# Optimization experiments

Hardware: AMD Instinct MI355X
Metric: run time of the kernel (lower is better)

Reference implementation:

```python
import jax, jax.numpy as jnp
import numpy as np

N_HEAD = 16

def setup_inputs() -> dict:
    key = jax.random.key(0)
    ks = jax.random.split(key, 5)
    B, S, D = 4, 2048, 1024
    return {
        "string": jax.random.normal(ks[0], (B, S, D), dtype=jnp.float32),
        "string_len": jax.random.randint(ks[1], (B,), 1, S + 1),
        "Wqkv": jax.random.normal(ks[2], (D, 3 * D), dtype=jnp.float32) * 0.02,
        "bqkv": jnp.zeros((3 * D,), dtype=jnp.float32),
        "Wo": jax.random.normal(ks[3], (D, D), dtype=jnp.float32) * 0.02,
        "bo": jnp.zeros((D,), dtype=jnp.float32),
    }


def reference(string, string_len, Wqkv, bqkv, Wo, bo):
    B, S, D = string.shape
    H = N_HEAD
    hd = D // H
    x = string @ Wqkv + bqkv                      # [B,S,3D]
    q, k, v = jnp.split(x, 3, axis=-1)
    # split heads -> [B,H,S,hd]
    q = q.reshape(B, S, H, hd).transpose(0, 2, 1, 3)
    k = k.reshape(B, S, H, hd).transpose(0, 2, 1, 3)
    v = v.reshape(B, S, H, hd).transpose(0, 2, 1, 3)
    w = jnp.einsum('bhqd,bhkd->bhqk', q, k) / jnp.sqrt(jnp.float32(hd))
    causal = jnp.tril(jnp.ones((S, S), dtype=bool))  # [S,S]
    w = jnp.where(causal[None, None], w, jnp.float32(-1e9))
    w = jax.nn.softmax(w, axis=-1)
    a = jnp.einsum('bhqk,bhkd->bhqd', w, v)       # [B,H,S,hd]
    a = a.transpose(0, 2, 1, 3).reshape(B, S, D)  # merge heads
    a = a @ Wo + bo
    return a, string_len
```

## Files before the change

### kernel.cpp

```cpp
#include <hip/hip_runtime.h>
#include <stdint.h>

typedef __attribute__((ext_vector_type(8))) short bf16x8;
typedef __attribute__((ext_vector_type(4))) float f32x4;
typedef __attribute__((ext_vector_type(16))) float f32x16;
typedef __attribute__((ext_vector_type(4))) unsigned short u16x4;

static constexpr int Bn = 4, Sn = 2048, Dn = 1024, Hn = 16, HD = 64;
static constexpr int Mrows = Bn * Sn;
static constexpr int D3 = 3 * Dn;

__device__ __forceinline__ unsigned short f2bf(float f) {
  unsigned int u = __float_as_uint(f);
  u += 0x7FFF + ((u >> 16) & 1);
  return (unsigned short)(u >> 16);
}

__device__ __forceinline__ void gload16(const void* gptr, void* lptr) {
  __builtin_amdgcn_global_load_lds(
      (__attribute__((address_space(1))) void*)gptr,
      (__attribute__((address_space(3))) void*)lptr, 16, 0, 0);
}

__device__ __forceinline__ int swz8(int r) { return (r ^ (r >> 3)) & 7; }

__device__ __forceinline__ float vexp2(float x) {
#if __has_builtin(__builtin_amdgcn_exp2f)
  return __builtin_amdgcn_exp2f(x);
#else
  return exp2f(x);
#endif
}

__device__ __forceinline__ unsigned cvtpk(float lo, float hi) {
  unsigned r;
  asm("v_cvt_pk_bf16_f32 %0, %1, %2" : "=v"(r) : "v"(lo), "v"(hi));
  return r;
}

__device__ __forceinline__ float lanepull(float v, int srclane) {
  return __int_as_float(__builtin_amdgcn_ds_bpermute(srclane * 4, __float_as_int(v)));
}

__global__ void cvt_f32_bf16(const float* __restrict__ in,
                             unsigned short* __restrict__ out, int n) {
  int i = (blockIdx.x * blockDim.x + threadIdx.x) * 4;
  if (i < n) {
    const float4 v = *(const float4*)(in + i);
    u16x4 o;
    o.x = f2bf(v.x); o.y = f2bf(v.y); o.z = f2bf(v.z); o.w = f2bf(v.w);
    *(u16x4*)(out + i) = o;
  }
}

__global__ void transpose_cvt(const float* __restrict__ W,
                              unsigned short* __restrict__ Wt, int K, int N) {
  __shared__ float tile[32][33];
  const int n0 = blockIdx.x * 32, k0 = blockIdx.y * 32;
  const int tx = threadIdx.x, ty = threadIdx.y;
  #pragma unroll
  for (int j = 0; j < 4; j++)
    tile[ty + 8 * j][tx] = W[(size_t)(k0 + ty + 8 * j) * N + n0 + tx];
  __syncthreads();
  #pragma unroll
  for (int j = 0; j < 4; j++)
    Wt[(size_t)(n0 + ty + 8 * j) * K + k0 + tx] = f2bf(tile[tx][ty + 8 * j]);
}

template<bool BF16_OUT>
__global__ __launch_bounds__(512, 1)
void gemm_bt2(const unsigned short* __restrict__ A,
              const unsigned short* __restrict__ Bt,
              const float* __restrict__ bias,
              void* __restrict__ Cout, int Nt, int Kt) {
  __shared__ __align__(128) unsigned char smem[98304];
  const int tid = threadIdx.x;
  const int w = tid >> 6, lane = tid & 63;
  const int wm = w >> 2, wn = w & 3;
  const int lrow = lane & 15, lk = lane >> 4;
  const long brow = (long)blockIdx.x * 128;
  const long bcol = (long)blockIdx.y * 256;

  const int srow = tid >> 3;
  const int sslot = tid & 7;

  auto stage = [&](int k0, unsigned char* buf) {
    unsigned char* Ab = buf;
    unsigned char* Bb = buf + 16384;
    #pragma unroll
    for (int i = 0; i < 2; i++) {
      const int r = srow + 64 * i;
      gload16(A + (size_t)(brow + r) * Kt + k0 + ((sslot ^ swz8(r)) * 8),
              Ab + w * 1024 + i * 8192);
    }
    #pragma unroll
    for (int i = 0; i < 4; i++) {
      const int r = srow + 64 * i;
      gload16(Bt + (size_t)(bcol + r) * Kt + k0 + ((sslot ^ swz8(r)) * 8),
              Bb + w * 1024 + i * 8192);
    }
  };

  f32x4 acc[4][4] = {};

  stage(0, smem);

  const int ntile = Kt >> 6;
  for (int t = 0; t < ntile; t++) {
    const int cur = t & 1;
    unsigned char* Ab = smem + cur * 49152;
    unsigned char* Bb = Ab + 16384;

    __builtin_amdgcn_s_barrier();
    if (t + 1 < ntile) {
      stage((t + 1) << 6, smem + (cur ^ 1) * 49152);
      asm volatile("s_waitcnt vmcnt(6)");
    } else {
      asm volatile("s_waitcnt vmcnt(0)");
    }
    __builtin_amdgcn_sched_barrier(0);
    __builtin_amdgcn_s_barrier();

    bf16x8 af[4][2], bfv[4][2];
    #pragma unroll
    for (int mt = 0; mt < 4; mt++) {
      const int r = wm * 64 + mt * 16 + lrow;
      #pragma unroll
      for (int kk = 0; kk < 2; kk++)
        af[mt][kk] = *(const bf16x8*)(Ab + r * 128 + (((kk * 4 + lk) ^ swz8(r)) * 16));
    }
    #pragma unroll
    for (int nt = 0; nt < 4; nt++) {
      const int r = wn * 64 + nt * 16 + lrow;
      #pragma unroll
      for (int kk = 0; kk < 2; kk++)
        bfv[nt][kk] = *(const bf16x8*)(Bb + r * 128 + (((kk * 4 + lk) ^ swz8(r)) * 16));
    }
    __builtin_amdgcn_s_setprio(1);
    #pragma unroll
    for (int mt = 0; mt < 4; mt++)
      #pragma unroll
      for (int nt = 0; nt < 4; nt++) {
        acc[mt][nt] = __builtin_amdgcn_mfma_f32_16x16x32_bf16(af[mt][0], bfv[nt][0], acc[mt][nt], 0, 0, 0);
        acc[mt][nt] = __builtin_amdgcn_mfma_f32_16x16x32_bf16(af[mt][1], bfv[nt][1], acc[mt][nt], 0, 0, 0);
      }
    __builtin_amdgcn_s_setprio(0);
  }

  #pragma unroll
  for (int nt = 0; nt < 4; nt++) {
    const long col = bcol + wn * 64 + nt * 16 + lrow;
    const float bv = bias[col];
    #pragma unroll
    for (int mt = 0; mt < 4; mt++) {
      #pragma unroll
      for (int rr = 0; rr < 4; rr++) {
        const long row = brow + wm * 64 + mt * 16 + lk * 4 + rr;
        const float v = acc[mt][nt][rr] + bv;
        if (BF16_OUT)
          ((unsigned short*)Cout)[row * Nt + col] = f2bf(v);
        else
          ((float*)Cout)[row * Nt + col] = v;
      }
    }
  }
}

__global__ __launch_bounds__(512, 2)
void attn_fwd2(const unsigned short* __restrict__ QKV,
               unsigned short* __restrict__ Out) {
  __shared__ __align__(128) unsigned char smem[65536];
  const int tid  = threadIdx.x;
  const int w    = tid >> 6;
  const int lane = tid & 63;
  const int li = lane & 31, hi = lane >> 5;
  const int bh = blockIdx.x;
  const int b  = bh >> 4, h = bh & 15;
  const int yy = (int)blockIdx.y;
  const int j  = (yy & 1) ? (yy >> 1) : (7 - (yy >> 1));
  const int wq = j * 256 + w * 32;
  const int qrow = wq + li;

  bf16x8 qf[4];
  {
    const unsigned short* qp = QKV + (size_t)(b * Sn + qrow) * D3 + h * HD + hi * 8;
    #pragma unroll
    for (int ks = 0; ks < 4; ks++) qf[ks] = *(const bf16x8*)(qp + ks * 16);
  }

  f32x16 o0 = {}, o1 = {};
  float m = -3.0e38f, lsum = 0.f;
  const float cexp = 0.18033688011112042f;

  auto kstage = [&](int kb, unsigned char* Kb) {
    #pragma unroll
    for (int i = 0; i < 2; i++) {
      const int r    = w * 16 + i * 8 + (lane >> 3);
      const int slot = (lane & 7) ^ swz8(r);
      gload16(QKV + (size_t)(b * Sn + kb + r) * D3 + Dn + h * HD + slot * 8,
              Kb + w * 2048 + i * 1024);
    }
  };
  const int vkv8 = tid >> 3;
  const int vd0  = (tid & 7) * 8;
  auto vload = [&](int kb, int i) -> bf16x8 {
    return *(const bf16x8*)(QKV + (size_t)(b * Sn + kb + i * 64 + vkv8) * D3 + 2 * Dn + h * HD + vd0);
  };
  auto vwrite = [&](bf16x8 vv, int i, unsigned char* Vb) {
    const int kv = i * 64 + vkv8;
    #pragma unroll
    for (int jj2 = 0; jj2 < 8; jj2++) {
      const int d  = vd0 + jj2;
      const int vs = (d ^ (d >> 3)) & 15;
      *(unsigned short*)(Vb + d * 256 + (((kv >> 3) ^ vs) << 4) + (kv & 7) * 2) = (unsigned short)vv[jj2];
    }
  };

  auto substep = [&](int s, int kb, const unsigned char* Kb, const unsigned char* Vb) {
    f32x16 s0 = {}, s1 = {};
    const int r0 = s * 64 + li, r1 = s * 64 + 32 + li;
    __builtin_amdgcn_s_setprio(1);
    #pragma unroll
    for (int ks = 0; ks < 4; ks++) {
      const int slot = ks * 2 + hi;
      const bf16x8 k0 = *(const bf16x8*)(Kb + r0 * 128 + ((slot ^ swz8(r0)) * 16));
      const bf16x8 k1 = *(const bf16x8*)(Kb + r1 * 128 + ((slot ^ swz8(r1)) * 16));
      s0 = __builtin_amdgcn_mfma_f32_32x32x16_bf16(k0, qf[ks], s0, 0, 0, 0);
      s1 = __builtin_amdgcn_mfma_f32_32x32x16_bf16(k1, qf[ks], s1, 0, 0, 0);
    }
    __builtin_amdgcn_s_setprio(0);
    const int kbase = kb + s * 64;
    if (kbase + 63 > wq) {
      #pragma unroll
      for (int r = 0; r < 16; r++) {
        const int kvl = (r & 3) + 8 * (r >> 2) + 4 * hi;
        if (kbase + kvl > qrow)      s0[r] = -3.0e38f;
        if (kbase + 32 + kvl > qrow) s1[r] = -3.0e38f;
      }
    }
    float t8[8];
    #pragma unroll
    for (int r = 0; r < 8; r++)
      t8[r] = fmaxf(fmaxf(s0[r], s0[r + 8]), fmaxf(s1[r], s1[r + 8]));
    float tmax = fmaxf(fmaxf(fmaxf(t8[0], t8[1]), fmaxf(t8[2], t8[3])),
                       fmaxf(fmaxf(t8[4], t8[5]), fmaxf(t8[6], t8[7])));
    tmax = fmaxf(tmax, __shfl_xor(tmax, 32));
    if (__any(tmax > m + 44.0f)) {
      const float mn   = fmaxf(m, tmax);
      const float corr = vexp2((m - mn) * cexp);
      m = mn;
      lsum *= corr;
      #pragma unroll
      for (int r = 0; r < 16; r++) {
        const float cr = lanepull(corr, (r & 3) + 8 * (r >> 2) + 4 * hi);
        o0[r] *= cr; o1[r] *= cr;
      }
    }
    const float mc = m * cexp;
    f32x16 p0, p1;
    float psa = 0.f, psb = 0.f, psc = 0.f, psd = 0.f;
    #pragma unroll
    for (int r = 0; r < 16; r += 4) {
      p0[r] = vexp2(fmaf(s0[r], cexp, -mc));         psa += p0[r];
      p0[r + 1] = vexp2(fmaf(s0[r + 1], cexp, -mc)); psb += p0[r + 1];
      p0[r + 2] = vexp2(fmaf(s0[r + 2], cexp, -mc)); psc += p0[r + 2];
      p0[r + 3] = vexp2(fmaf(s0[r + 3], cexp, -mc)); psd += p0[r + 3];
    }
    #pragma unroll
    for (int r = 0; r < 16; r += 4) {
      p1[r] = vexp2(fmaf(s1[r], cexp, -mc));         psa += p1[r];
      p1[r + 1] = vexp2(fmaf(s1[r + 1], cexp, -mc)); psb += p1[r + 1];
      p1[r + 2] = vexp2(fmaf(s1[r + 2], cexp, -mc)); psc += p1[r + 2];
      p1[r + 3] = vexp2(fmaf(s1[r + 3], cexp, -mc)); psd += p1[r + 3];
    }
    lsum += (psa + psb) + (psc + psd);

    auto mk_pa = [&](const f32x16& pp, int base) -> bf16x8 {
      const unsigned a0 = cvtpk(pp[base + 0], pp[base + 1]);
      const unsigned a1 = cvtpk(pp[base + 2], pp[base + 3]);
      const unsigned b0 = cvtpk(pp[base + 4], pp[base + 5]);
      const unsigned b1 = cvtpk(pp[base + 6], pp[base + 7]);
      const unsigned xa0 = __shfl_xor(a0, 32), xa1 = __shfl_xor(a1, 32);
      const unsigned xb0 = __shfl_xor(b0, 32), xb1 = __shfl_xor(b1, 32);
      union { unsigned u[4]; bf16x8 v; } pu;
      pu.u[0] = hi ? xb0 : a0;
      pu.u[1] = hi ? xb1 : a1;
      pu.u[2] = hi ? b0  : xa0;
      pu.u[3] = hi ? b1  : xa1;
      return pu.v;
    };
    bf16x8 pa[4];
    pa[0] = mk_pa(p0, 0); pa[1] = mk_pa(p0, 8);
    pa[2] = mk_pa(p1, 0); pa[3] = mk_pa(p1, 8);

    const int vs0 = (li ^ (li >> 3)) & 15;
    const int vs1 = ((32 + li) ^ ((32 + li) >> 3)) & 15;
    __builtin_amdgcn_s_setprio(1);
    #pragma unroll
    for (int k16 = 0; k16 < 4; k16++) {
      const int slot = s * 8 + k16 * 2 + hi;
      const bf16x8 vb0 = *(const bf16x8*)(Vb + li * 256 + ((slot ^ vs0) << 4));
      const bf16x8 vb1 = *(const bf16x8*)(Vb + (32 + li) * 256 + ((slot ^ vs1) << 4));
      o0 = __builtin_amdgcn_mfma_f32_32x32x16_bf16(pa[k16], vb0, o0, 0, 0, 0);
      o1 = __builtin_amdgcn_mfma_f32_32x32x16_bf16(pa[k16], vb1, o1, 0, 0, 0);
    }
    __builtin_amdgcn_s_setprio(0);
  };

  kstage(0, smem);
  {
    bf16x8 va = vload(0, 0), vb = vload(0, 1);
    vwrite(va, 0, smem + 16384);
    vwrite(vb, 1, smem + 16384);
  }
  asm volatile("s_waitcnt lgkmcnt(0)");
  __builtin_amdgcn_sched_barrier(0);

  const int nt = 2 * j + 2;
  for (int t = 0; t < nt; t++) {
    const int kb  = t << 7;
    const int cur = t & 1;
    unsigned char* Kb = smem + cur * 32768;
    unsigned char* Vb = Kb + 16384;
    const bool pre = (t + 1 < nt);
    bf16x8 vna, vnb;

    __builtin_amdgcn_s_barrier();
    if (pre) {
      kstage(kb + 128, smem + (cur ^ 1) * 32768);
      vna = vload(kb + 128, 0);
      vnb = vload(kb + 128, 1);
    }

    if (kb <= wq + 31) {
      substep(0, kb, Kb, Vb);
      if (kb + 64 <= wq + 31) substep(1, kb, Kb, Vb);
    }

    if (pre) {
      unsigned char* Vn = smem + (cur ^ 1) * 32768 + 16384;
      vwrite(vna, 0, Vn);
      vwrite(vnb, 1, Vn);
    }
    asm volatile("s_waitcnt lgkmcnt(0)");
    __builtin_amdgcn_sched_barrier(0);
  }

  const float lt = lsum + __shfl_xor(lsum, 32);
  const float rl = __builtin_amdgcn_rcpf(lt);
  #pragma unroll
  for (int r = 0; r < 16; r++) {
    const int q = (r & 3) + 8 * (r >> 2) + 4 * hi;
    const float rr = lanepull(rl, q);
    unsigned short* op = Out + (size_t)(b * Sn + wq + q) * Dn + h * HD;
    op[li]      = f2bf(o0[r] * rr);
    op[32 + li] = f2bf(o1[r] * rr);
  }
}

__global__ void copy_len(const int* __restrict__ slen, float* __restrict__ dst, int n) {
  const int i = threadIdx.x;
  if (i < n) dst[i] = (float)slen[i];
}

extern "C" void kernel_launch(void* const* d_in, const int* in_sizes, int n_in,
                              void* d_out, int out_size, void* d_ws, size_t ws_size,
                              hipStream_t stream) {
  const float* X    = (const float*)d_in[0];
  const int*   slen = (const int*)d_in[1];
  const float* Wqkv = (const float*)d_in[2];
  const float* bqkv = (const float*)d_in[3];
  const float* Wo   = (const float*)d_in[4];
  const float* bo   = (const float*)d_in[5];
  float* out = (float*)d_out;

  char* ws = (char*)d_ws;
  unsigned short* Xb    = (unsigned short*)ws;
  unsigned short* Wtq   = (unsigned short*)(ws + 16777216);
  unsigned short* Wto   = (unsigned short*)(ws + 16777216 + 6291456);
  unsigned short* QKVb  = (unsigned short*)(ws + 16777216 + 6291456 + 2097152);
  unsigned short* Attnb = Xb;

  cvt_f32_bf16<<<dim3(8192), dim3(256), 0, stream>>>(X, Xb, Mrows * Dn);
  transpose_cvt<<<dim3(96, 32), dim3(32, 8), 0, stream>>>(Wqkv, Wtq, Dn, D3);
  transpose_cvt<<<dim3(32, 32), dim3(32, 8), 0, stream>>>(Wo, Wto, Dn, Dn);

  gemm_bt2<true><<<dim3(64, 12), dim3(512), 0, stream>>>(Xb, Wtq, bqkv, (void*)QKVb, D3, Dn);
  attn_fwd2<<<dim3(64, 8), dim3(512), 0, stream>>>(QKVb, Attnb);
  gemm_bt2<false><<<dim3(64, 4), dim3(512), 0, stream>>>(Attnb, Wto, bo, d_out, Dn, Dn);
  copy_len<<<dim3(1), dim3(64), 0, stream>>>(slen, out + (size_t)Mrows * Dn, Bn);
}
```

Baseline: 187.9 us.

## Pair high and low causal query tiles per block to share K/V loads

The attention kernel now processes two query tiles per block, one from the high end and one from the low end of the causal range, so every block does the same amount of work. Each K/V tile staged into shared memory is reused by both query tiles, which halves the number of blocks and removes redundant K/V loads for the low tile. The cost is twice the accumulator and Q register state per thread, with launch bounds dropped to one block per CU, which lowers occupancy and may cause register spills.

```diff
diff --git a/kernel.cpp b/kernel.cpp
--- a/kernel.cpp
+++ b/kernel.cpp
@@ -166,8 +166,8 @@
   }
 }
 
-__global__ __launch_bounds__(512, 2)
-void attn_fwd2(const unsigned short* __restrict__ QKV,
+__global__ __launch_bounds__(512, 1)
+void attn_pair(const unsigned short* __restrict__ QKV,
                unsigned short* __restrict__ Out) {
   __shared__ __align__(128) unsigned char smem[65536];
   const int tid  = threadIdx.x;
@@ -176,21 +176,26 @@
   const int li = lane & 31, hi = lane >> 5;
   const int bh = blockIdx.x;
   const int b  = bh >> 4, h = bh & 15;
-  const int yy = (int)blockIdx.y;
-  const int j  = (yy & 1) ? (yy >> 1) : (7 - (yy >> 1));
-  const int wq = j * 256 + w * 32;
-  const int qrow = wq + li;
-
-  bf16x8 qf[4];
+  const int p  = blockIdx.y;
+  const int wqh = (7 - p) * 256 + w * 32;
+  const int wql = p * 256 + w * 32;
+
+  const float cexp = 0.18033688011112042f;
+
+  bf16x8 qfh[4], qfl[4];
   {
-    const unsigned short* qp = QKV + (size_t)(b * Sn + qrow) * D3 + h * HD + hi * 8;
-    #pragma unroll
-    for (int ks = 0; ks < 4; ks++) qf[ks] = *(const bf16x8*)(qp + ks * 16);
-  }
-
-  f32x16 o0 = {}, o1 = {};
-  float m = -3.0e38f, lsum = 0.f;
-  const float cexp = 0.18033688011112042f;
+    const unsigned short* qp = QKV + (size_t)(b * Sn + wqh + li) * D3 + h * HD + hi * 8;
+    #pragma unroll
+    for (int ks = 0; ks < 4; ks++) qfh[ks] = *(const bf16x8*)(qp + ks * 16);
+  }
+  {
+    const unsigned short* qp = QKV + (size_t)(b * Sn + wql + li) * D3 + h * HD + hi * 8;
+    #pragma unroll
+    for (int ks = 0; ks < 4; ks++) qfl[ks] = *(const bf16x8*)(qp + ks * 16);
+  }
+
+  f32x16 o0h = {}, o1h = {}, o0l = {}, o1l = {};
+  float mh = -3.0e38f, lsh = 0.f, ml = -3.0e38f, lsl = 0.f;
 
   auto kstage = [&](int kb, unsigned char* Kb) {
     #pragma unroll
@@ -209,14 +214,17 @@
   auto vwrite = [&](bf16x8 vv, int i, unsigned char* Vb) {
     const int kv = i * 64 + vkv8;
     #pragma unroll
-    for (int jj2 = 0; jj2 < 8; jj2++) {
-      const int d  = vd0 + jj2;
+    for (int jj = 0; jj < 8; jj++) {
+      const int d  = vd0 + jj;
       const int vs = (d ^ (d >> 3)) & 15;
-      *(unsigned short*)(Vb + d * 256 + (((kv >> 3) ^ vs) << 4) + (kv & 7) * 2) = (unsigned short)vv[jj2];
+      *(unsigned short*)(Vb + d * 256 + (((kv >> 3) ^ vs) << 4) + (kv & 7) * 2) = (unsigned short)vv[jj];
     }
   };
 
-  auto substep = [&](int s, int kb, const unsigned char* Kb, const unsigned char* Vb) {
+  auto substep = [&](int s, int kb, const unsigned char* Kb, const unsigned char* Vb,
+                     int wqX, bf16x8 (&qf)[4], f32x16& o0, f32x16& o1,
+                     float& m, float& ls) {
+    const int qrowX = wqX + li;
     f32x16 s0 = {}, s1 = {};
     const int r0 = s * 64 + li, r1 = s * 64 + 32 + li;
     __builtin_amdgcn_s_setprio(1);
@@ -230,12 +238,12 @@
     }
     __builtin_amdgcn_s_setprio(0);
     const int kbase = kb + s * 64;
-    if (kbase + 63 > wq) {
+    if (kbase + 63 > wqX) {
       #pragma unroll
       for (int r = 0; r < 16; r++) {
         const int kvl = (r & 3) + 8 * (r >> 2) + 4 * hi;
-        if (kbase + kvl > qrow)      s0[r] = -3.0e38f;
-        if (kbase + 32 + kvl > qrow) s1[r] = -3.0e38f;
+        if (kbase + kvl > qrowX)      s0[r] = -3.0e38f;
+        if (kbase + 32 + kvl > qrowX) s1[r] = -3.0e38f;
       }
     }
     float t8[8];
@@ -249,7 +257,7 @@
       const float mn   = fmaxf(m, tmax);
       const float corr = vexp2((m - mn) * cexp);
       m = mn;
-      lsum *= corr;
+      ls *= corr;
       #pragma unroll
       for (int r = 0; r < 16; r++) {
         const float cr = lanepull(corr, (r & 3) + 8 * (r >> 2) + 4 * hi);
@@ -273,7 +281,7 @@
       p1[r + 2] = vexp2(fmaf(s1[r + 2], cexp, -mc)); psc += p1[r + 2];
       p1[r + 3] = vexp2(fmaf(s1[r + 3], cexp, -mc)); psd += p1[r + 3];
     }
-    lsum += (psa + psb) + (psc + psd);
+    ls += (psa + psb) + (psc + psd);
 
     auto mk_pa = [&](const f32x16& pp, int base) -> bf16x8 {
       const unsigned a0 = cvtpk(pp[base + 0], pp[base + 1]);
@@ -316,7 +324,7 @@
   asm volatile("s_waitcnt lgkmcnt(0)");
   __builtin_amdgcn_sched_barrier(0);
 
-  const int nt = 2 * j + 2;
+  const int nt = 16 - 2 * p;
   for (int t = 0; t < nt; t++) {
     const int kb  = t << 7;
     const int cur = t & 1;
@@ -332,9 +340,13 @@
       vnb = vload(kb + 128, 1);
     }
 
-    if (kb <= wq + 31) {
-      substep(0, kb, Kb, Vb);
-      if (kb + 64 <= wq + 31) substep(1, kb, Kb, Vb);
+    if (kb <= wqh + 31) {
+      substep(0, kb, Kb, Vb, wqh, qfh, o0h, o1h, mh, lsh);
+      if (kb + 64 <= wqh + 31) substep(1, kb, Kb, Vb, wqh, qfh, o0h, o1h, mh, lsh);
+    }
+    if (kb <= wql + 31) {
+      substep(0, kb, Kb, Vb, wql, qfl, o0l, o1l, ml, lsl);
+      if (kb + 64 <= wql + 31) substep(1, kb, Kb, Vb, wql, qfl, o0l, o1l, ml, lsl);
     }
 
     if (pre) {
@@ -346,15 +358,29 @@
     __builtin_amdgcn_sched_barrier(0);
   }
 
-  const float lt = lsum + __shfl_xor(lsum, 32);
-  const float rl = __builtin_amdgcn_rcpf(lt);
-  #pragma unroll
-  for (int r = 0; r < 16; r++) {
-    const int q = (r & 3) + 8 * (r >> 2) + 4 * hi;
-    const float rr = lanepull(rl, q);
-    unsigned short* op = Out + (size_t)(b * Sn + wq + q) * Dn + h * HD;
-    op[li]      = f2bf(o0[r] * rr);
-    op[32 + li] = f2bf(o1[r] * rr);
+  {
+    const float lt = lsh + __shfl_xor(lsh, 32);
+    const float rl = __builtin_amdgcn_rcpf(lt);
+    #pragma unroll
+    for (int r = 0; r < 16; r++) {
+      const int q = (r & 3) + 8 * (r >> 2) + 4 * hi;
+      const float rr = lanepull(rl, q);
+      unsigned short* op = Out + (size_t)(b * Sn + wqh + q) * Dn + h * HD;
+      op[li]      = f2bf(o0h[r] * rr);
+      op[32 + li] = f2bf(o1h[r] * rr);
+    }
+  }
+  {
+    const float lt = lsl + __shfl_xor(lsl, 32);
+    const float rl = __builtin_amdgcn_rcpf(lt);
+    #pragma unroll
+    for (int r = 0; r < 16; r++) {
+      const int q = (r & 3) + 8 * (r >> 2) + 4 * hi;
+      const float rr = lanepull(rl, q);
+      unsigned short* op = Out + (size_t)(b * Sn + wql + q) * Dn + h * HD;
+      op[li]      = f2bf(o0l[r] * rr);
+      op[32 + li] = f2bf(o1l[r] * rr);
+    }
   }
 }
 
@@ -386,7 +412,7 @@
   transpose_cvt<<<dim3(32, 32), dim3(32, 8), 0, stream>>>(Wo, Wto, Dn, Dn);
 
   gemm_bt2<true><<<dim3(64, 12), dim3(512), 0, stream>>>(Xb, Wtq, bqkv, (void*)QKVb, D3, Dn);
-  attn_fwd2<<<dim3(64, 8), dim3(512), 0, stream>>>(QKVb, Attnb);
+  attn_pair<<<dim3(64, 4), dim3(512), 0, stream>>>(QKVb, Attnb);
   gemm_bt2<false><<<dim3(64, 4), dim3(512), 0, stream>>>(Attnb, Wto, bo, d_out, Dn, Dn);
   copy_len<<<dim3(1), dim3(64), 0, stream>>>(slen, out + (size_t)Mrows * Dn, Bn);
 }
```

New measurement: 177.6 us. 5.5% less time.
